# Kernel tuning notes

Hardware: AMD Instinct MI355X
Metric: run time of the kernel (lower is better)

The kernel has to match this reference:

```python
import jax, jax.numpy as jnp
import numpy as np

N_NODES = 100000
N_EDGES = 1600000
D = 128  # in_features


def setup_inputs() -> dict:
    key = jax.random.key(0)
    k1, k2, k3 = jax.random.split(key, 3)
    node_embeddings = jax.random.normal(k1, (N_NODES, D), dtype=jnp.float32)
    edge_index = jax.random.randint(k2, (2, N_EDGES), 0, N_NODES, dtype=jnp.int64)
    # attn_fc: Linear(2*D, 2) -> weight [2, 2*D], bias [2]
    W = jax.random.normal(k3, (2, 2 * D), dtype=jnp.float32) * (1.0 / np.sqrt(2 * D))
    b = jnp.zeros((2,), dtype=jnp.float32)
    return {"node_embeddings": node_embeddings, "edge_index": edge_index, "W": W, "b": b}


def reference(node_embeddings, edge_index, W, b):
    # Gather endpoint embeddings per edge, concat -> [E, 2*D]
    row, col = edge_index[0], edge_index[1]
    edge_feature = jnp.concatenate(
        [node_embeddings[row], node_embeddings[col]], axis=-1
    )  # [E, 2D]
    attn_scores = edge_feature @ W.T + b  # [E, 2]
    attn_scores = jax.nn.softmax(attn_scores, axis=-1)
    # dropout is identity in eval mode
    return attn_scores
```

## Files before the change

### kernel.cpp

```cpp
#include <hip/hip_runtime.h>

static constexpr int kNodes = 100000;
static constexpr int kEdges = 1600000;
static constexpr int kD     = 128;

typedef float fx4 __attribute__((ext_vector_type(4)));

__global__ __launch_bounds__(256) void node_pre(const float* __restrict__ emb,
                                                const float* __restrict__ W,
                                                float* __restrict__ uv) {
    const int l  = threadIdx.x & 15;
    const int c0 = l * 8;

    fx4 w0a = *(const fx4*)&W[c0],       w0b = *(const fx4*)&W[c0 + 4];
    fx4 w1a = *(const fx4*)&W[256 + c0], w1b = *(const fx4*)&W[256 + c0 + 4];
    fx4 dua = w1a - w0a, dub = w1b - w0b;
    fx4 w2a = *(const fx4*)&W[128 + c0], w2b = *(const fx4*)&W[128 + c0 + 4];
    fx4 w3a = *(const fx4*)&W[384 + c0], w3b = *(const fx4*)&W[384 + c0 + 4];
    fx4 dva = w3a - w2a, dvb = w3b - w2b;

    const int n = (blockIdx.x * blockDim.x + threadIdx.x) >> 4;
    if (n >= kNodes) return;

    const fx4* row = (const fx4*)(emb + (size_t)n * kD + c0);
    fx4 ea = row[0];
    fx4 eb = row[1];

    float pu = ea.x*dua.x + ea.y*dua.y + ea.z*dua.z + ea.w*dua.w
             + eb.x*dub.x + eb.y*dub.y + eb.z*dub.z + eb.w*dub.w;
    float pv = ea.x*dva.x + ea.y*dva.y + ea.z*dva.z + ea.w*dva.w
             + eb.x*dvb.x + eb.y*dvb.y + eb.z*dvb.z + eb.w*dvb.w;

    float keep = (l & 1) ? pv : pu;
    float send = (l & 1) ? pu : pv;
    float x = keep + __shfl_xor(send, 1);
    x += __shfl_xor(x, 2);
    x += __shfl_xor(x, 4);
    x += __shfl_xor(x, 8);

    if (l < 2) uv[n * 2 + l] = x;
}

__global__ __launch_bounds__(256) void edge_attn(const void* __restrict__ eiv,
                                                 const float* __restrict__ uv,
                                                 const float* __restrict__ b,
                                                 float* __restrict__ out) {
    const unsigned long long* ei64 = (const unsigned long long*)eiv;
    unsigned long long hi = ei64[threadIdx.x & 63] >> 32;
    const bool is64 = (__ballot(hi != 0ull) == 0ull);

    const int e2 = blockIdx.x * blockDim.x + threadIdx.x;
    if (e2 >= kEdges / 2) return;

    int r0, r1, c0i, c1i;
    if (is64) {
        const unsigned long long* rr = ei64 + 2 * e2;
        const unsigned long long* cc = ei64 + kEdges + 2 * e2;
        r0  = (int)rr[0]; r1  = (int)rr[1];
        c0i = (int)cc[0]; c1i = (int)cc[1];
    } else {
        const int* ei32 = (const int*)eiv;
        r0  = ei32[2 * e2];          r1  = ei32[2 * e2 + 1];
        c0i = ei32[kEdges + 2 * e2]; c1i = ei32[kEdges + 2 * e2 + 1];
    }

    const float db = b[1] - b[0];

    float d0 = uv[2 * r0] + uv[2 * c0i + 1] + db;
    float d1 = uv[2 * r1] + uv[2 * c1i + 1] + db;

    float p00 = __builtin_amdgcn_rcpf(1.0f + __expf(d0));
    float p10 = __builtin_amdgcn_rcpf(1.0f + __expf(d1));

    fx4 o = {p00, 1.0f - p00, p10, 1.0f - p10};
    ((fx4*)out)[e2] = o;
}

extern "C" void kernel_launch(void* const* d_in, const int* in_sizes, int n_in,
                              void* d_out, int out_size, void* d_ws, size_t ws_size,
                              hipStream_t stream) {
    const float* emb = (const float*)d_in[0];
    const void*  ei  = d_in[1];
    const float* W   = (const float*)d_in[2];
    const float* b   = (const float*)d_in[3];
    float* out = (float*)d_out;

    float* uv = (float*)d_ws;

    node_pre<<<(kNodes * 16 + 255) / 256, 256, 0, stream>>>(emb, W, uv);

    edge_attn<<<(kEdges / 2 + 255) / 256, 256, 0, stream>>>(ei, uv, b, out);
}
```

Baseline: 32.54 us.

## Fuse node and edge kernels into one persistent kernel with grid barrier

Replaces the two launches with a single persistent kernel of 1024 blocks. It first computes per-node projections with a grid-stride loop, prefetches the edge indices into registers, waits at a two-level atomic grid barrier, and then runs the edge softmax. The goal is to remove the second launch and the gap between kernels, and to overlap the index loads with the node phase. In exchange it adds a memset launch to clear the barrier flags, and it relies on all 1024 blocks being resident at once, which could deadlock if occupancy is insufficient.

```diff
diff --git a/kernel.cpp b/kernel.cpp
--- a/kernel.cpp
+++ b/kernel.cpp
@@ -1,17 +1,147 @@
 #include <hip/hip_runtime.h>
 
-static constexpr int kNodes = 100000;
-static constexpr int kEdges = 1600000;
-static constexpr int kD     = 128;
-
-typedef float fx4 __attribute__((ext_vector_type(4)));
+static constexpr int kNodes   = 100000;
+static constexpr int kEdges   = 1600000;
+static constexpr int kPairs   = kEdges / 2;
+static constexpr int kD       = 128;
+static constexpr int kBlocks  = 1024;
+static constexpr int kThreads = kBlocks * 256;
+static constexpr int kLeaves  = 16;
+static constexpr int kQuota   = kBlocks / kLeaves;
+
+typedef float              fx4 __attribute__((ext_vector_type(4)));
+typedef unsigned long long u64;
+
+__device__ inline void grid_barrier(u64* __restrict__ leaves,
+                                    u64* __restrict__ root) {
+    __syncthreads();
+    if (threadIdx.x == 0) {
+        const int leaf = blockIdx.x & (kLeaves - 1);
+        u64 old = __hip_atomic_fetch_add(&leaves[leaf * 16], 1ull,
+                                         __ATOMIC_RELEASE,
+                                         __HIP_MEMORY_SCOPE_AGENT);
+        if (old == (u64)(kQuota - 1)) {
+            __hip_atomic_fetch_add(root, 1ull, __ATOMIC_RELEASE,
+                                   __HIP_MEMORY_SCOPE_AGENT);
+        }
+        while (__hip_atomic_load(root, __ATOMIC_RELAXED,
+                                 __HIP_MEMORY_SCOPE_AGENT) < (u64)kLeaves) {
+            __builtin_amdgcn_s_sleep(8);
+        }
+        __builtin_amdgcn_fence(__ATOMIC_ACQUIRE, "agent");
+    }
+    __syncthreads();
+}
+
+__global__ __launch_bounds__(256, 4) void fused(const float* __restrict__ emb,
+                                                const void* __restrict__ eiv,
+                                                const float* __restrict__ W,
+                                                const float* __restrict__ b,
+                                                u64* __restrict__ flags,
+                                                float* __restrict__ uv,
+                                                float* __restrict__ out) {
+    const int tid = blockIdx.x * 256 + threadIdx.x;
+    const int l   = threadIdx.x & 15;
+    const int c0  = l * 8;
+
+    {
+        fx4 w0a = *(const fx4*)&W[c0],       w0b = *(const fx4*)&W[c0 + 4];
+        fx4 w1a = *(const fx4*)&W[256 + c0], w1b = *(const fx4*)&W[256 + c0 + 4];
+        fx4 dua = w1a - w0a, dub = w1b - w0b;
+        fx4 w2a = *(const fx4*)&W[128 + c0], w2b = *(const fx4*)&W[128 + c0 + 4];
+        fx4 w3a = *(const fx4*)&W[384 + c0], w3b = *(const fx4*)&W[384 + c0 + 4];
+        fx4 dva = w3a - w2a, dvb = w3b - w2b;
+
+        const int group   = tid >> 4;
+        const int ngroups = kThreads >> 4;
+        for (int n = group; n < kNodes; n += ngroups) {
+            const fx4* row = (const fx4*)(emb + (size_t)n * kD + c0);
+            fx4 ea = row[0];
+            fx4 eb = row[1];
+            float pu = ea.x*dua.x + ea.y*dua.y + ea.z*dua.z + ea.w*dua.w
+                     + eb.x*dub.x + eb.y*dub.y + eb.z*dub.z + eb.w*dub.w;
+            float pv = ea.x*dva.x + ea.y*dva.y + ea.z*dva.z + ea.w*dva.w
+                     + eb.x*dvb.x + eb.y*dvb.y + eb.z*dvb.z + eb.w*dvb.w;
+            float keep = (l & 1) ? pv : pu;
+            float send = (l & 1) ? pu : pv;
+            float x = keep + __shfl_xor(send, 1);
+            x += __shfl_xor(x, 2);
+            x += __shfl_xor(x, 4);
+            x += __shfl_xor(x, 8);
+            if (l < 2) uv[n * 2 + l] = x;
+        }
+    }
+
+    const u64* ei64 = (const u64*)eiv;
+    u64 hi = ei64[threadIdx.x & 63] >> 32;
+    const bool is64 = (__ballot(hi != 0ull) == 0ull);
+
+    const float db = b[1] - b[0];
+    u64* root = flags + 15 * 16 + 16;
+
+    if (is64) {
+        u64 rbuf[8], cbuf[8];
+#pragma unroll
+        for (int k = 0; k < 4; ++k) {
+            int p = tid + k * kThreads;
+            if (p < kPairs) {
+                rbuf[2*k]   = ei64[2 * p];
+                rbuf[2*k+1] = ei64[2 * p + 1];
+                cbuf[2*k]   = ei64[kEdges + 2 * p];
+                cbuf[2*k+1] = ei64[kEdges + 2 * p + 1];
+            }
+        }
+        grid_barrier(flags, root);
+#pragma unroll
+        for (int k = 0; k < 4; ++k) {
+            int p = tid + k * kThreads;
+            if (p < kPairs) {
+                int r0 = (int)rbuf[2*k], r1 = (int)rbuf[2*k+1];
+                int cc0 = (int)cbuf[2*k], cc1 = (int)cbuf[2*k+1];
+                float d0 = uv[2 * r0] + uv[2 * cc0 + 1] + db;
+                float d1 = uv[2 * r1] + uv[2 * cc1 + 1] + db;
+                float p00 = __builtin_amdgcn_rcpf(1.0f + __expf(d0));
+                float p10 = __builtin_amdgcn_rcpf(1.0f + __expf(d1));
+                fx4 o = {p00, 1.0f - p00, p10, 1.0f - p10};
+                ((fx4*)out)[p] = o;
+            }
+        }
+    } else {
+        const int* ei32 = (const int*)eiv;
+        int rbuf[8], cbuf[8];
+#pragma unroll
+        for (int k = 0; k < 4; ++k) {
+            int p = tid + k * kThreads;
+            if (p < kPairs) {
+                rbuf[2*k]   = ei32[2 * p];
+                rbuf[2*k+1] = ei32[2 * p + 1];
+                cbuf[2*k]   = ei32[kEdges + 2 * p];
+                cbuf[2*k+1] = ei32[kEdges + 2 * p + 1];
+            }
+        }
+        grid_barrier(flags, root);
+#pragma unroll
+        for (int k = 0; k < 4; ++k) {
+            int p = tid + k * kThreads;
+            if (p < kPairs) {
+                int r0 = rbuf[2*k], r1 = rbuf[2*k+1];
+                int cc0 = cbuf[2*k], cc1 = cbuf[2*k+1];
+                float d0 = uv[2 * r0] + uv[2 * cc0 + 1] + db;
+                float d1 = uv[2 * r1] + uv[2 * cc1 + 1] + db;
+                float p00 = __builtin_amdgcn_rcpf(1.0f + __expf(d0));
+                float p10 = __builtin_amdgcn_rcpf(1.0f + __expf(d1));
+                fx4 o = {p00, 1.0f - p00, p10, 1.0f - p10};
+                ((fx4*)out)[p] = o;
+            }
+        }
+    }
+}
 
 __global__ __launch_bounds__(256) void node_pre(const float* __restrict__ emb,
                                                 const float* __restrict__ W,
                                                 float* __restrict__ uv) {
     const int l  = threadIdx.x & 15;
     const int c0 = l * 8;
-
     fx4 w0a = *(const fx4*)&W[c0],       w0b = *(const fx4*)&W[c0 + 4];
     fx4 w1a = *(const fx4*)&W[256 + c0], w1b = *(const fx4*)&W[256 + c0 + 4];
     fx4 dua = w1a - w0a, dub = w1b - w0b;
@@ -21,23 +151,19 @@
 
     const int n = (blockIdx.x * blockDim.x + threadIdx.x) >> 4;
     if (n >= kNodes) return;
-
     const fx4* row = (const fx4*)(emb + (size_t)n * kD + c0);
     fx4 ea = row[0];
     fx4 eb = row[1];
-
     float pu = ea.x*dua.x + ea.y*dua.y + ea.z*dua.z + ea.w*dua.w
              + eb.x*dub.x + eb.y*dub.y + eb.z*dub.z + eb.w*dub.w;
     float pv = ea.x*dva.x + ea.y*dva.y + ea.z*dva.z + ea.w*dva.w
              + eb.x*dvb.x + eb.y*dvb.y + eb.z*dvb.z + eb.w*dvb.w;
-
     float keep = (l & 1) ? pv : pu;
     float send = (l & 1) ? pu : pv;
     float x = keep + __shfl_xor(send, 1);
     x += __shfl_xor(x, 2);
     x += __shfl_xor(x, 4);
     x += __shfl_xor(x, 8);
-
     if (l < 2) uv[n * 2 + l] = x;
 }
 
@@ -45,33 +171,27 @@
                                                  const float* __restrict__ uv,
                                                  const float* __restrict__ b,
                                                  float* __restrict__ out) {
-    const unsigned long long* ei64 = (const unsigned long long*)eiv;
-    unsigned long long hi = ei64[threadIdx.x & 63] >> 32;
+    const u64* ei64 = (const u64*)eiv;
+    u64 hi = ei64[threadIdx.x & 63] >> 32;
     const bool is64 = (__ballot(hi != 0ull) == 0ull);
 
     const int e2 = blockIdx.x * blockDim.x + threadIdx.x;
-    if (e2 >= kEdges / 2) return;
+    if (e2 >= kPairs) return;
 
     int r0, r1, c0i, c1i;
     if (is64) {
-        const unsigned long long* rr = ei64 + 2 * e2;
-        const unsigned long long* cc = ei64 + kEdges + 2 * e2;
-        r0  = (int)rr[0]; r1  = (int)rr[1];
-        c0i = (int)cc[0]; c1i = (int)cc[1];
+        r0  = (int)ei64[2 * e2];          r1  = (int)ei64[2 * e2 + 1];
+        c0i = (int)ei64[kEdges + 2 * e2]; c1i = (int)ei64[kEdges + 2 * e2 + 1];
     } else {
         const int* ei32 = (const int*)eiv;
         r0  = ei32[2 * e2];          r1  = ei32[2 * e2 + 1];
         c0i = ei32[kEdges + 2 * e2]; c1i = ei32[kEdges + 2 * e2 + 1];
     }
-
     const float db = b[1] - b[0];
-
     float d0 = uv[2 * r0] + uv[2 * c0i + 1] + db;
     float d1 = uv[2 * r1] + uv[2 * c1i + 1] + db;
-
     float p00 = __builtin_amdgcn_rcpf(1.0f + __expf(d0));
     float p10 = __builtin_amdgcn_rcpf(1.0f + __expf(d1));
-
     fx4 o = {p00, 1.0f - p00, p10, 1.0f - p10};
     ((fx4*)out)[e2] = o;
 }
@@ -85,9 +205,14 @@
     const float* b   = (const float*)d_in[3];
     float* out = (float*)d_out;
 
-    float* uv = (float*)d_ws;
-
-    node_pre<<<(kNodes * 16 + 255) / 256, 256, 0, stream>>>(emb, W, uv);
-
-    edge_attn<<<(kEdges / 2 + 255) / 256, 256, 0, stream>>>(ei, uv, b, out);
-}
+    u64*   flags = (u64*)d_ws;
+    float* uv    = (float*)((char*)d_ws + 8192);
+
+    hipError_t err = hipMemsetAsync(d_ws, 0, 4096, stream);
+    if (err == hipSuccess) {
+        fused<<<kBlocks, 256, 0, stream>>>(emb, ei, W, b, flags, uv, out);
+    } else {
+        node_pre<<<(kNodes * 16 + 255) / 256, 256, 0, stream>>>(emb, W, uv);
+        edge_attn<<<(kPairs + 255) / 256, 256, 0, stream>>>(ei, uv, b, out);
+    }
+}
```

After: 60.21 us. 1.85x slower.
